# Optimization experiments

Hardware: AMD Instinct MI355X
Metric: run time of the kernel (lower is better)

Reference implementation:

```python
import jax, jax.numpy as jnp
import numpy as np

NUM_HEADS = 8  # from init_kwargs


def setup_inputs() -> dict:
    key = jax.random.key(0)
    ks = jax.random.split(key, 8)
    B, N, Din, H, Dout, E = 4, 2048, 256, 512, 256, 65536
    s = 0.02
    return {
        "x": jax.random.normal(ks[0], (B, N, Din), jnp.float32),
        "edge_index": jax.random.randint(ks[1], (2, E), 0, N),
        "W_gcn": jax.random.normal(ks[2], (Din, H), jnp.float32) * s,
        "b_gcn": jnp.zeros((H,), jnp.float32),
        "in_proj_w": jax.random.normal(ks[3], (3 * H, H), jnp.float32) * s,
        "in_proj_b": jnp.zeros((3 * H,), jnp.float32),
        "out_proj_w": jax.random.normal(ks[4], (H, H), jnp.float32) * s,
        "out_proj_b": jnp.zeros((H,), jnp.float32),
        "fc_w": jax.random.normal(ks[5], (H, Dout), jnp.float32) * s,
        "fc_b": jnp.zeros((Dout,), jnp.float32),
    }


def _gcn(x, edge_index, W, b):
    # PyG GCNConv: add self-loops, symmetric normalization, gather-scatter aggregation.
    B, N, _ = x.shape
    loop = jnp.arange(N)
    src = jnp.concatenate([edge_index[0], loop])  # message source j
    dst = jnp.concatenate([edge_index[1], loop])  # aggregation target i
    deg = jnp.zeros((N,), x.dtype).at[dst].add(1.0)
    dinv = jnp.where(deg > 0, jax.lax.rsqrt(deg), 0.0)
    norm = dinv[src] * dinv[dst]                  # [Etot]
    xl = x @ W                                    # [B, N, H]
    msgs = xl[:, src, :] * norm[None, :, None]    # [B, Etot, H]
    out = jnp.zeros_like(xl).at[:, dst].add(msgs)  # scatter-add over edges
    return out + b


def _mha(x_nbh, wi, bi, wo, bo, nh):
    # torch MultiheadAttention, input [N(seq), B, H], self-attention.
    N, B, H = x_nbh.shape
    dh = H // nh
    qkv = x_nbh @ wi.T + bi                       # [N, B, 3H]
    q, k, v = jnp.split(qkv, 3, axis=-1)
    q = q.reshape(N, B, nh, dh) * (dh ** -0.5)
    k = k.reshape(N, B, nh, dh)
    v = v.reshape(N, B, nh, dh)
    scores = jnp.einsum("nbhd,mbhd->bhnm", q, k)  # [B, nh, N, N]
    attn = jax.nn.softmax(scores, axis=-1)
    o = jnp.einsum("bhnm,mbhd->nbhd", attn, v).reshape(N, B, H)
    return o @ wo.T + bo


def reference(x, edge_index, W_gcn, b_gcn, in_proj_w, in_proj_b,
              out_proj_w, out_proj_b, fc_w, fc_b):
    h = _gcn(x, edge_index, W_gcn, b_gcn)         # [B, N, H]
    h = jnp.transpose(h, (1, 0, 2))               # [N, B, H]
    h = _mha(h, in_proj_w, in_proj_b, out_proj_w, out_proj_b, NUM_HEADS)
    h = jnp.transpose(h, (1, 0, 2))               # [B, N, H]
    h = jax.nn.relu(h)
    return h @ fc_w + fc_b                        # [B, N, Dout]
```

## Files before the change

### kernel.cpp

```cpp
#include <hip/hip_runtime.h>
#include <hip/hip_bf16.h>


#define NN 2048
#define HH 512
#define NHEAD 8
#define DH 64

typedef _Float16 f16;
typedef __attribute__((ext_vector_type(2))) _Float16 f16x2;
typedef __attribute__((ext_vector_type(4))) _Float16 f16x4;
typedef __attribute__((ext_vector_type(8))) _Float16 f16x8;
typedef __attribute__((ext_vector_type(4))) float f32x4;

#define GLOAD_LDS16(g, l)                                              \
  __builtin_amdgcn_global_load_lds(                                    \
      (const __attribute__((address_space(1))) void*)(g),              \
      (__attribute__((address_space(3))) void*)(l), 16, 0, 0)

__device__ __forceinline__ float fast_exp2(float x) {
#if __has_builtin(__builtin_amdgcn_exp2f)
  return __builtin_amdgcn_exp2f(x);
#else
  return exp2f(x);
#endif
}

__device__ __forceinline__ f16x2 cvt_pk_f16(float a, float b) {
#if __has_builtin(__builtin_amdgcn_cvt_pkrtz)
  return __builtin_bit_cast(f16x2, __builtin_amdgcn_cvt_pkrtz(a, b));
#else
  f16x2 r = { (f16)a, (f16)b };
  return r;
#endif
}


__global__ __launch_bounds__(256) void prep_all_kernel(const float* __restrict__ wi,
                                                       const float* __restrict__ wo,
                                                       const float* __restrict__ wg,
                                                       const float* __restrict__ fcw,
                                                       f16* __restrict__ wi16,
                                                       f16* __restrict__ wo16,
                                                       f16* __restrict__ wg16t,
                                                       f16* __restrict__ fcw16t,
                                                       float* __restrict__ deg,
                                                       int* __restrict__ cursor) {
  __shared__ float tbuf[32][33];
  const int bid = blockIdx.x, t = threadIdx.x;
  if (bid < 768) {
    const int i = bid * 256 + t;
    const float4 v = ((const float4*)wi)[i];
    f16x4 o = { (f16)v.x, (f16)v.y, (f16)v.z, (f16)v.w };
    ((f16x4*)wi16)[i] = o;
  } else if (bid < 1024) {
    const int i = (bid - 768) * 256 + t;
    const float4 v = ((const float4*)wo)[i];
    f16x4 o = { (f16)v.x, (f16)v.y, (f16)v.z, (f16)v.w };
    ((f16x4*)wo16)[i] = o;
  } else if (bid == 1024) {
    for (int i = t; i < NN; i += 256) { deg[i] = 0.0f; cursor[i] = 0; }
  } else {
    const int id = bid - 1025;
    const float* in;
    f16* outp;
    int R, C, bx, by;
    if (id < 128) { in = wg;  outp = wg16t;  R = 256; C = 512;
                    bx = id & 15; by = id >> 4; }
    else { int id2 = id - 128; in = fcw; outp = fcw16t; R = 512; C = 256;
           bx = id2 & 7; by = id2 >> 3; }
    const int c0 = bx * 32, r0 = by * 32;
    const int tx = t & 31, ty = t >> 5;
#pragma unroll
    for (int i = 0; i < 32; i += 8) tbuf[ty + i][tx] = in[(size_t)(r0 + ty + i) * C + c0 + tx];
    __syncthreads();
#pragma unroll
    for (int i = 0; i < 32; i += 8)
      outp[(size_t)(c0 + ty + i) * R + r0 + tx] = (f16)tbuf[tx][ty + i];
  }
}


__global__ __launch_bounds__(256) void count_deg_kernel(const int* __restrict__ ei, int E,
                                                        float* __restrict__ deg) {
  int e = blockIdx.x * 256 + threadIdx.x;
  if (e < E) atomicAdd(&deg[ei[E + e]], 1.0f);
}

__global__ __launch_bounds__(1024) void build_rowptr_kernel(const float* __restrict__ deg,
                                                            float* __restrict__ dinv,
                                                            int* __restrict__ rowptr) {
  __shared__ int a[NN];
  __shared__ int bbuf[NN];
  const int t = threadIdx.x;
  for (int i = t; i < NN; i += 1024) {
    float dg = deg[i];
    a[i] = (int)dg;
    dinv[i] = rsqrtf(dg + 1.0f);
  }
  __syncthreads();
  int* src = a;
  int* dst = bbuf;
  for (int off = 1; off < NN; off <<= 1) {
    for (int i = t; i < NN; i += 1024) {
      int v = src[i];
      if (i >= off) v += src[i - off];
      dst[i] = v;
    }
    __syncthreads();
    int* tmp = src; src = dst; dst = tmp;
  }
  for (int i = t; i < NN; i += 1024) rowptr[i + 1] = src[i];
  if (t == 0) rowptr[0] = 0;
}

__global__ __launch_bounds__(256) void fill_csr_kernel(const int* __restrict__ ei, int E,
                                                       const int* __restrict__ rowptr,
                                                       int* __restrict__ cursor,
                                                       int* __restrict__ csr_src) {
  int e = blockIdx.x * 256 + threadIdx.x;
  if (e < E) {
    int s = ei[e];
    int d = ei[E + e];
    int pos = atomicAdd(&cursor[d], 1);
    csr_src[rowptr[d] + pos] = s;
  }
}


template <int OUTMODE, bool BIAS, bool RELU, bool AF32, int MT = 128>
__global__ __launch_bounds__(256) void mfma_gemm_kernel(
    const void* __restrict__ Ap, const f16* __restrict__ Bt,
    const float* __restrict__ bias, void* __restrict__ Cout,
    int M, int N, int K,
    f16* __restrict__ q_out, f16* __restrict__ k_out, f16* __restrict__ v_out) {
  constexpr int MI = MT / 32;
  __shared__ f16 As[MT * 32];
  __shared__ f16 Bs[128 * 32];
  const int tid = threadIdx.x;
  const int wave = tid >> 6, lane = tid & 63;
  const int quad = lane >> 4, l16 = lane & 15;
  const int m0 = blockIdx.y * MT, n0 = blockIdx.x * 128;
  const int moff = (wave >> 1) * (MI * 16), noff = (wave & 1) * 64;

  f32x4 acc[MI][4];
#pragma unroll
  for (int i = 0; i < MI; ++i)
#pragma unroll
    for (int j = 0; j < 4; ++j) acc[i][j] = (f32x4){0.f, 0.f, 0.f, 0.f};

  const int rpw = MT / 4;
  const int srowA = rpw * wave + (lane >> 2);
  const int srowB = 32 * wave + (lane >> 2);
  const int kch = (lane & 3) * 8;
  const f16* Ag = (const f16*)Ap + (size_t)(m0 + srowA) * K + kch;
  const float* Ag32 = (const float*)Ap + (size_t)(m0 + srowA) * K + kch;
  const f16* Bg = Bt + (size_t)(n0 + srowB) * K + kch;
  f16* As_w = &As[(rpw * wave) * 32];
  f16* Bs_w = &Bs[(32 * wave) * 32];

  for (int k0 = 0; k0 < K; k0 += 32) {
    __syncthreads();
    if (AF32) {
#pragma unroll
      for (int t = 0; t < 2; ++t) {
        const float* g = Ag32 + k0 + (size_t)(16 * t) * K;
        const float4 u0 = *(const float4*)g;
        const float4 u1 = *(const float4*)(g + 4);
        f16x8 o = { (f16)u0.x, (f16)u0.y, (f16)u0.z, (f16)u0.w,
                    (f16)u1.x, (f16)u1.y, (f16)u1.z, (f16)u1.w };
        *(f16x8*)&As[(srowA + 16 * t) * 32 + kch] = o;
      }
    } else {
      GLOAD_LDS16(Ag + k0, As_w);
      if (MT == 128) GLOAD_LDS16(Ag + k0 + (size_t)16 * K, As_w + 16 * 32);
    }
    GLOAD_LDS16(Bg + k0, Bs_w);
    GLOAD_LDS16(Bg + k0 + (size_t)16 * K, Bs_w + 16 * 32);
    __syncthreads();
    f16x8 af[MI], bf[4];
#pragma unroll
    for (int m16 = 0; m16 < MI; ++m16)
      af[m16] = *(const f16x8*)&As[(moff + m16 * 16 + l16) * 32 + quad * 8];
#pragma unroll
    for (int n16 = 0; n16 < 4; ++n16)
      bf[n16] = *(const f16x8*)&Bs[(noff + n16 * 16 + l16) * 32 + quad * 8];
#pragma unroll
    for (int m16 = 0; m16 < MI; ++m16)
#pragma unroll
      for (int n16 = 0; n16 < 4; ++n16)
        acc[m16][n16] =
            __builtin_amdgcn_mfma_f32_16x16x32_f16(af[m16], bf[n16], acc[m16][n16], 0, 0, 0);
  }

  float bv[4];
#pragma unroll
  for (int n16 = 0; n16 < 4; ++n16)
    bv[n16] = BIAS ? bias[n0 + noff + n16 * 16 + l16] : 0.f;

  if (OUTMODE == 2) {
    const int hblk = (n0 >> 6) + (wave & 1);
    const int which = hblk >> 3, h = hblk & 7;
    f16* dst = (which == 0) ? q_out : (which == 1) ? k_out : v_out;
    const float scale = (which == 0) ? 0.125f * 1.44269504088896340736f : 1.0f;
#pragma unroll
    for (int m16 = 0; m16 < MI; ++m16) {
#pragma unroll
      for (int r = 0; r < 4; ++r) {
        const int m = m0 + moff + m16 * 16 + quad * 4 + r;
        const int b = m >> 11, ns = m & 2047;
        f16* row = dst + ((size_t)(b * 8 + h) * NN + ns) * DH;
#pragma unroll
        for (int n16 = 0; n16 < 4; ++n16) {
          const int d = n16 * 16 + l16;
          row[d] = (f16)((acc[m16][n16][r] + bv[n16]) * scale);
        }
      }
    }
  } else {
#pragma unroll
    for (int m16 = 0; m16 < MI; ++m16) {
#pragma unroll
      for (int r = 0; r < 4; ++r) {
        const size_t row = (size_t)(m0 + moff + m16 * 16 + quad * 4 + r) * N;
#pragma unroll
        for (int n16 = 0; n16 < 4; ++n16) {
          const int col = n0 + noff + n16 * 16 + l16;
          float v = acc[m16][n16][r] + bv[n16];
          if (RELU) v = fmaxf(v, 0.f);
          if (OUTMODE == 0) ((float*)Cout)[row + col] = v;
          else ((f16*)Cout)[row + col] = (f16)v;
        }
      }
    }
  }
}


__global__ __launch_bounds__(256) void gcn_aggregate_kernel(const f16* __restrict__ xl,
                                                            const float* __restrict__ dinv,
                                                            const int* __restrict__ rowptr,
                                                            const int* __restrict__ csr_src,
                                                            const float* __restrict__ b_gcn,
                                                            f16* __restrict__ out) {
  __shared__ int s_src[256];
  __shared__ float s_dv[256];
  const int i = blockIdx.x;
  const int tid = threadIdx.x;
  const float dv_i = dinv[i];
  const int b = tid >> 6;
  const int f = (tid & 63) * 8;
  const f16* xb = xl + (size_t)(b * NN) * HH + f;
  float acc[8];
  {
    const f16x8 self = *(const f16x8*)&xb[(size_t)i * HH];
#pragma unroll
    for (int j = 0; j < 8; ++j) acc[j] = (float)self[j] * dv_i;
  }
  const int beg = rowptr[i], end = rowptr[i + 1];
  for (int c0 = beg; c0 < end; c0 += 256) {
    const int cnt = min(256, end - c0);
    __syncthreads();
    if (tid < cnt) {
      int s = csr_src[c0 + tid];
      s_src[tid] = s;
      s_dv[tid] = dinv[s];
    }
    __syncthreads();
    for (int t = 0; t < cnt; ++t) {
      const f16x8 v = *(const f16x8*)&xb[(size_t)s_src[t] * HH];
      const float w = s_dv[t];
#pragma unroll
      for (int j = 0; j < 8; ++j) acc[j] = fmaf((float)v[j], w, acc[j]);
    }
  }
  const float4 bg0 = *(const float4*)&b_gcn[f];
  const float4 bg1 = *(const float4*)&b_gcn[f + 4];
  f16x8 o;
  o[0] = (f16)(acc[0] * dv_i + bg0.x);
  o[1] = (f16)(acc[1] * dv_i + bg0.y);
  o[2] = (f16)(acc[2] * dv_i + bg0.z);
  o[3] = (f16)(acc[3] * dv_i + bg0.w);
  o[4] = (f16)(acc[4] * dv_i + bg1.x);
  o[5] = (f16)(acc[5] * dv_i + bg1.y);
  o[6] = (f16)(acc[6] * dv_i + bg1.z);
  o[7] = (f16)(acc[7] * dv_i + bg1.w);
  *(f16x8*)&out[((size_t)(b * NN) + i) * HH + f] = o;
}


__global__ __launch_bounds__(512) void flash_attn_f16_kernel(const f16* __restrict__ Qb,
                                                             const f16* __restrict__ Kb,
                                                             const f16* __restrict__ Vb,
                                                             f16* __restrict__ out) {
  constexpr int LDK = 72;
  constexpr int LDV = 128;
  __shared__ f16 Ks[2][128 * LDK];
  __shared__ f16 Vt[2][64 * LDV];
  const int tid = threadIdx.x;
  const int wave = tid >> 6, lane = tid & 63;
  const int quad = lane >> 4, l16 = lane & 15;
  const int bid = blockIdx.x;
  const int sw = (bid & 7) * 64 + (bid >> 3);
  const int bh = sw >> 4;
  const int n0 = (sw & 15) * 128;
  const int b = bh >> 3, h = bh & 7;
  const f16* kb = Kb + (size_t)bh * NN * DH;
  const f16* vb = Vb + (size_t)bh * NN * DH;

  f16x8 aq0, aq1;
  {
    const f16* qf = Qb + ((size_t)bh * NN + n0 + wave * 16 + l16) * DH + quad * 8;
    aq0 = *(const f16x8*)qf;
    aq1 = *(const f16x8*)(qf + 32);
  }

  float l_part = 0.f;
  f32x4 acc_o[4];
#pragma unroll
  for (int n16 = 0; n16 < 4; ++n16) acc_o[n16] = (f32x4){0.f, 0.f, 0.f, 0.f};

  const int krow = tid >> 3, kcol = (tid & 7) * 8;
  const int vdg = tid & 15, jb = tid >> 4;
  const int vch = (jb >> 3) * 4 + (jb & 3);
  const int vrem = ((jb >> 2) & 1) * 4;
  int fdr[4];
#pragma unroll
  for (int n16 = 0; n16 < 4; ++n16)
    fdr[n16] = (2 * n16 + l16 + (l16 >> 3)) & 7;

  f16x8 kreg0, kreg1;
  f16x4 vreg[4];

  auto load_tile = [&](int k0) {
    kreg0 = *(const f16x8*)(kb + (size_t)(k0 + krow) * DH + kcol);
    kreg1 = *(const f16x8*)(kb + (size_t)(k0 + 64 + krow) * DH + kcol);
#pragma unroll
    for (int i = 0; i < 4; ++i)
      vreg[i] = *(const f16x4*)(vb + (size_t)(k0 + jb * 4 + i) * DH + vdg * 4);
  };
  auto store_tile = [&](int buf) {
    *(f16x8*)&Ks[buf][krow * LDK + kcol] = kreg0;
    *(f16x8*)&Ks[buf][(64 + krow) * LDK + kcol] = kreg1;
#pragma unroll
    for (int c = 0; c < 4; ++c) {
      const int d = vdg * 4 + c;
      const int fd = (d + (d >> 3)) & 7;
      const int off = (((vch & 8) | ((vch ^ fd) & 7)) << 3) + vrem;
      f16x4 o = { vreg[0][c], vreg[1][c], vreg[2][c], vreg[3][c] };
      *(f16x4*)&Vt[buf][d * LDV + off] = o;
    }
  };
  auto do_p = [&](int p, int cur) {
    const f16* KsC = &Ks[cur][0];
    const f16* VtC = &Vt[cur][0];
    f32x4 sA[2];
#pragma unroll
    for (int t = 0; t < 2; ++t) {
      const f16x8 ak0 = *(const f16x8*)&KsC[(p * 32 + t * 16 + l16) * LDK + quad * 8];
      const f16x8 ak1 = *(const f16x8*)&KsC[(p * 32 + t * 16 + l16) * LDK + quad * 8 + 32];
      f32x4 s = {0.f, 0.f, 0.f, 0.f};
      s = __builtin_amdgcn_mfma_f32_16x16x32_f16(ak0, aq0, s, 0, 0, 0);
      s = __builtin_amdgcn_mfma_f32_16x16x32_f16(ak1, aq1, s, 0, 0, 0);
      sA[t] = s;
    }
    f16x8 bvv[4];
    const int chp = p * 4 + quad;
#pragma unroll
    for (int n16 = 0; n16 < 4; ++n16) {
      const int off = ((chp & 8) | ((chp ^ fdr[n16]) & 7)) << 3;
      bvv[n16] = *(const f16x8*)&VtC[(n16 * 16 + l16) * LDV + off];
    }
    union { f16x8 v; f16x2 hh[4]; } ap;
    float sum = 0.f;
#pragma unroll
    for (int t = 0; t < 2; ++t)
#pragma unroll
      for (int rr = 0; rr < 2; ++rr) {
        const float e0 = fast_exp2(sA[t][rr * 2]);
        const float e1 = fast_exp2(sA[t][rr * 2 + 1]);
        sum += e0 + e1;
        ap.hh[t * 2 + rr] = cvt_pk_f16(e0, e1);
      }
    l_part += sum;
#pragma unroll
    for (int n16 = 0; n16 < 4; ++n16)
      acc_o[n16] = __builtin_amdgcn_mfma_f32_16x16x32_f16(ap.v, bvv[n16], acc_o[n16], 0, 0, 0);
  };

  load_tile(0);
  store_tile(0);
  int cur = 0;
  for (int kt = 0; kt < NN / 128; ++kt) {
    __syncthreads();
    const bool pf = (kt + 1) < (NN / 128);
    if (pf) load_tile((kt + 1) * 128);
    do_p(0, cur);
    do_p(1, cur);
    if (pf) store_tile(cur ^ 1);
    do_p(2, cur);
    do_p(3, cur);
    cur ^= 1;
  }

  float lp = l_part;
  lp += __shfl_xor(lp, 16);
  lp += __shfl_xor(lp, 32);
  f16* obase = out + ((size_t)b * NN + n0 + wave * 16) * HH + h * DH;
#pragma unroll
  for (int r = 0; r < 4; ++r) {
    const float lr = __shfl(lp, (lane & 48) | (quad * 4 + r));
    const float inv = 1.0f / lr;
#pragma unroll
    for (int n16 = 0; n16 < 4; ++n16)
      obase[(size_t)(quad * 4 + r) * HH + n16 * 16 + l16] = (f16)(acc_o[n16][r] * inv);
  }
}


extern "C" void kernel_launch(void* const* d_in, const int* in_sizes, int n_in,
                              void* d_out, int out_size, void* d_ws, size_t ws_size,
                              hipStream_t stream) {
  const float* x     = (const float*)d_in[0];
  const int*   ei    = (const int*)d_in[1];
  const float* W_gcn = (const float*)d_in[2];
  const float* b_gcn = (const float*)d_in[3];
  const float* wi    = (const float*)d_in[4];
  const float* bi    = (const float*)d_in[5];
  const float* wo    = (const float*)d_in[6];
  const float* bo    = (const float*)d_in[7];
  const float* fcw   = (const float*)d_in[8];
  const float* fcb   = (const float*)d_in[9];
  float* out = (float*)d_out;
  const int E = in_sizes[1] / 2;
  const int M = 4 * NN;

  char* wsb = (char*)d_ws;
  const size_t MB = 1u << 20;
  f16* xl16   = (f16*)(wsb + 4 * MB);
  f16* hb16   = (f16*)(wsb + 12 * MB);
  f16* Qb     = (f16*)(wsb + 20 * MB);
  f16* Kb     = (f16*)(wsb + 28 * MB);
  f16* Vb     = (f16*)(wsb + 36 * MB);
  f16* attn16 = (f16*)(wsb + 44 * MB);
  f16* proj16 = (f16*)(wsb + 52 * MB);
  f16* wi16   = (f16*)(wsb + 60 * MB);
  f16* wo16   = (f16*)(wsb + 62 * MB);
  f16* wg16t  = (f16*)(wsb + 63 * MB);
  f16* fcw16t = (f16*)(wsb + 64 * MB);
  float* deg  = (float*)(wsb + 65 * MB);
  float* dinv = deg + NN;
  int* rowptr = (int*)(dinv + NN);
  int* cursor = rowptr + 2080;
  int* csr    = cursor + NN;

  prep_all_kernel<<<1281, 256, 0, stream>>>(wi, wo, W_gcn, fcw, wi16, wo16,
                                            wg16t, fcw16t, deg, cursor);

  count_deg_kernel<<<(E + 255) / 256, 256, 0, stream>>>(ei, E, deg);
  build_rowptr_kernel<<<1, 1024, 0, stream>>>(deg, dinv, rowptr);
  fill_csr_kernel<<<(E + 255) / 256, 256, 0, stream>>>(ei, E, rowptr, cursor, csr);

  mfma_gemm_kernel<1, false, false, true><<<dim3(4, 64), 256, 0, stream>>>(
      x, wg16t, nullptr, xl16, M, 512, 256, nullptr, nullptr, nullptr);
  gcn_aggregate_kernel<<<NN, 256, 0, stream>>>(xl16, dinv, rowptr, csr, b_gcn, hb16);
  mfma_gemm_kernel<2, true, false, false><<<dim3(12, 64), 256, 0, stream>>>(
      hb16, wi16, bi, nullptr, M, 1536, 512, Qb, Kb, Vb);
  flash_attn_f16_kernel<<<512, 512, 0, stream>>>(Qb, Kb, Vb, attn16);
  mfma_gemm_kernel<1, true, true, false><<<dim3(4, 64), 256, 0, stream>>>(
      attn16, wo16, bo, proj16, M, 512, 512, nullptr, nullptr, nullptr);
  mfma_gemm_kernel<0, true, false, false, 64><<<dim3(2, 128), 256, 0, stream>>>(
      proj16, fcw16t, fcb, out, M, 256, 512, nullptr, nullptr, nullptr);
}
```

Before: 245.0 us.

## Halve attention block to 4 waves each handling two query groups, single-buffer LDS

The flash attention kernel now runs 256 threads per block, with each wave processing two 16-row query groups. Each K and V fragment read from LDS is reused across both groups, halving LDS reads per FLOP. LDS drops from double to single buffering, so the loop adds an extra barrier before each tile store. Wave priority is raised around the MFMA phase. The trade-offs are higher register pressure (two accumulator sets, with launch bounds asking for 2 blocks/SM) and less overlap between loads and compute.

```diff
diff --git a/kernel.cpp b/kernel.cpp
--- a/kernel.cpp
+++ b/kernel.cpp
@@ -289,14 +289,14 @@
 }
 
 
-__global__ __launch_bounds__(512) void flash_attn_f16_kernel(const f16* __restrict__ Qb,
-                                                             const f16* __restrict__ Kb,
-                                                             const f16* __restrict__ Vb,
-                                                             f16* __restrict__ out) {
+__global__ __launch_bounds__(256, 2) void flash_attn_f16_kernel(const f16* __restrict__ Qb,
+                                                                const f16* __restrict__ Kb,
+                                                                const f16* __restrict__ Vb,
+                                                                f16* __restrict__ out) {
   constexpr int LDK = 72;
   constexpr int LDV = 128;
-  __shared__ f16 Ks[2][128 * LDK];
-  __shared__ f16 Vt[2][64 * LDV];
+  __shared__ f16 Ks[128 * LDK];
+  __shared__ f16 Vt[64 * LDV];
   const int tid = threadIdx.x;
   const int wave = tid >> 6, lane = tid & 63;
   const int quad = lane >> 4, l16 = lane & 15;
@@ -308,112 +308,136 @@
   const f16* kb = Kb + (size_t)bh * NN * DH;
   const f16* vb = Vb + (size_t)bh * NN * DH;
 
-  f16x8 aq0, aq1;
-  {
-    const f16* qf = Qb + ((size_t)bh * NN + n0 + wave * 16 + l16) * DH + quad * 8;
-    aq0 = *(const f16x8*)qf;
-    aq1 = *(const f16x8*)(qf + 32);
-  }
-
-  float l_part = 0.f;
-  f32x4 acc_o[4];
-#pragma unroll
-  for (int n16 = 0; n16 < 4; ++n16) acc_o[n16] = (f32x4){0.f, 0.f, 0.f, 0.f};
-
-  const int krow = tid >> 3, kcol = (tid & 7) * 8;
-  const int vdg = tid & 15, jb = tid >> 4;
-  const int vch = (jb >> 3) * 4 + (jb & 3);
-  const int vrem = ((jb >> 2) & 1) * 4;
+  f16x8 aq[2][2];
+#pragma unroll
+  for (int g = 0; g < 2; ++g) {
+    const f16* qf = Qb + ((size_t)bh * NN + n0 + (wave + 4 * g) * 16 + l16) * DH + quad * 8;
+    aq[g][0] = *(const f16x8*)qf;
+    aq[g][1] = *(const f16x8*)(qf + 32);
+  }
+
+  float l_part[2] = {0.f, 0.f};
+  f32x4 acc_o[2][4];
+#pragma unroll
+  for (int g = 0; g < 2; ++g)
+#pragma unroll
+    for (int n16 = 0; n16 < 4; ++n16) acc_o[g][n16] = (f32x4){0.f, 0.f, 0.f, 0.f};
+
+  const int kr = tid >> 3, kc = (tid & 7) * 8;
+  const int vdg = tid & 15, jbb = tid >> 4;
   int fdr[4];
 #pragma unroll
   for (int n16 = 0; n16 < 4; ++n16)
     fdr[n16] = (2 * n16 + l16 + (l16 >> 3)) & 7;
 
-  f16x8 kreg0, kreg1;
-  f16x4 vreg[4];
+  f16x8 kreg[4];
+  f16x4 vreg[2][4];
 
   auto load_tile = [&](int k0) {
-    kreg0 = *(const f16x8*)(kb + (size_t)(k0 + krow) * DH + kcol);
-    kreg1 = *(const f16x8*)(kb + (size_t)(k0 + 64 + krow) * DH + kcol);
 #pragma unroll
     for (int i = 0; i < 4; ++i)
-      vreg[i] = *(const f16x4*)(vb + (size_t)(k0 + jb * 4 + i) * DH + vdg * 4);
+      kreg[i] = *(const f16x8*)(kb + (size_t)(k0 + kr + 32 * i) * DH + kc);
+#pragma unroll
+    for (int cc = 0; cc < 2; ++cc) {
+      const int jb = jbb + 16 * cc;
+#pragma unroll
+      for (int i = 0; i < 4; ++i)
+        vreg[cc][i] = *(const f16x4*)(vb + (size_t)(k0 + jb * 4 + i) * DH + vdg * 4);
+    }
   };
-  auto store_tile = [&](int buf) {
-    *(f16x8*)&Ks[buf][krow * LDK + kcol] = kreg0;
-    *(f16x8*)&Ks[buf][(64 + krow) * LDK + kcol] = kreg1;
-#pragma unroll
-    for (int c = 0; c < 4; ++c) {
-      const int d = vdg * 4 + c;
-      const int fd = (d + (d >> 3)) & 7;
-      const int off = (((vch & 8) | ((vch ^ fd) & 7)) << 3) + vrem;
-      f16x4 o = { vreg[0][c], vreg[1][c], vreg[2][c], vreg[3][c] };
-      *(f16x4*)&Vt[buf][d * LDV + off] = o;
+  auto store_tile = [&]() {
+#pragma unroll
+    for (int i = 0; i < 4; ++i)
+      *(f16x8*)&Ks[(kr + 32 * i) * LDK + kc] = kreg[i];
+#pragma unroll
+    for (int cc = 0; cc < 2; ++cc) {
+      const int jb = jbb + 16 * cc;
+      const int vch = (jb >> 3) * 4 + (jb & 3);
+      const int vrem = ((jb >> 2) & 1) * 4;
+#pragma unroll
+      for (int c = 0; c < 4; ++c) {
+        const int d = vdg * 4 + c;
+        const int fd = (d + (d >> 3)) & 7;
+        const int off = (((vch & 8) | ((vch ^ fd) & 7)) << 3) + vrem;
+        f16x4 o = { vreg[cc][0][c], vreg[cc][1][c], vreg[cc][2][c], vreg[cc][3][c] };
+        *(f16x4*)&Vt[d * LDV + off] = o;
+      }
     }
   };
-  auto do_p = [&](int p, int cur) {
-    const f16* KsC = &Ks[cur][0];
-    const f16* VtC = &Vt[cur][0];
-    f32x4 sA[2];
+  auto do_p = [&](int p) {
+    f32x4 sA[2][2];
 #pragma unroll
     for (int t = 0; t < 2; ++t) {
-      const f16x8 ak0 = *(const f16x8*)&KsC[(p * 32 + t * 16 + l16) * LDK + quad * 8];
-      const f16x8 ak1 = *(const f16x8*)&KsC[(p * 32 + t * 16 + l16) * LDK + quad * 8 + 32];
-      f32x4 s = {0.f, 0.f, 0.f, 0.f};
-      s = __builtin_amdgcn_mfma_f32_16x16x32_f16(ak0, aq0, s, 0, 0, 0);
-      s = __builtin_amdgcn_mfma_f32_16x16x32_f16(ak1, aq1, s, 0, 0, 0);
-      sA[t] = s;
+      const f16x8 ak0 = *(const f16x8*)&Ks[(p * 32 + t * 16 + l16) * LDK + quad * 8];
+      const f16x8 ak1 = *(const f16x8*)&Ks[(p * 32 + t * 16 + l16) * LDK + quad * 8 + 32];
+#pragma unroll
+      for (int g = 0; g < 2; ++g) {
+        f32x4 s = {0.f, 0.f, 0.f, 0.f};
+        s = __builtin_amdgcn_mfma_f32_16x16x32_f16(ak0, aq[g][0], s, 0, 0, 0);
+        s = __builtin_amdgcn_mfma_f32_16x16x32_f16(ak1, aq[g][1], s, 0, 0, 0);
+        sA[g][t] = s;
+      }
     }
     f16x8 bvv[4];
     const int chp = p * 4 + quad;
 #pragma unroll
     for (int n16 = 0; n16 < 4; ++n16) {
       const int off = ((chp & 8) | ((chp ^ fdr[n16]) & 7)) << 3;
-      bvv[n16] = *(const f16x8*)&VtC[(n16 * 16 + l16) * LDV + off];
-    }
-    union { f16x8 v; f16x2 hh[4]; } ap;
-    float sum = 0.f;
-#pragma unroll
-    for (int t = 0; t < 2; ++t)
-#pragma unroll
-      for (int rr = 0; rr < 2; ++rr) {
-        const float e0 = fast_exp2(sA[t][rr * 2]);
-        const float e1 = fast_exp2(sA[t][rr * 2 + 1]);
-        sum += e0 + e1;
-        ap.hh[t * 2 + rr] = cvt_pk_f16(e0, e1);
-      }
-    l_part += sum;
-#pragma unroll
-    for (int n16 = 0; n16 < 4; ++n16)
-      acc_o[n16] = __builtin_amdgcn_mfma_f32_16x16x32_f16(ap.v, bvv[n16], acc_o[n16], 0, 0, 0);
+      bvv[n16] = *(const f16x8*)&Vt[(n16 * 16 + l16) * LDV + off];
+    }
+#pragma unroll
+    for (int g = 0; g < 2; ++g) {
+      union { f16x8 v; f16x2 hh[4]; } ap;
+      float sum = 0.f;
+#pragma unroll
+      for (int t = 0; t < 2; ++t)
+#pragma unroll
+        for (int rr = 0; rr < 2; ++rr) {
+          const float e0 = fast_exp2(sA[g][t][rr * 2]);
+          const float e1 = fast_exp2(sA[g][t][rr * 2 + 1]);
+          sum += e0 + e1;
+          ap.hh[t * 2 + rr] = cvt_pk_f16(e0, e1);
+        }
+      l_part[g] += sum;
+#pragma unroll
+      for (int n16 = 0; n16 < 4; ++n16)
+        acc_o[g][n16] = __builtin_amdgcn_mfma_f32_16x16x32_f16(ap.v, bvv[n16], acc_o[g][n16], 0, 0, 0);
+    }
   };
 
   load_tile(0);
-  store_tile(0);
-  int cur = 0;
+  store_tile();
+  __syncthreads();
   for (int kt = 0; kt < NN / 128; ++kt) {
-    __syncthreads();
     const bool pf = (kt + 1) < (NN / 128);
     if (pf) load_tile((kt + 1) * 128);
-    do_p(0, cur);
-    do_p(1, cur);
-    if (pf) store_tile(cur ^ 1);
-    do_p(2, cur);
-    do_p(3, cur);
-    cur ^= 1;
-  }
-
-  float lp = l_part;
-  lp += __shfl_xor(lp, 16);
-  lp += __shfl_xor(lp, 32);
-  f16* obase = out + ((size_t)b * NN + n0 + wave * 16) * HH + h * DH;
-#pragma unroll
-  for (int r = 0; r < 4; ++r) {
-    const float lr = __shfl(lp, (lane & 48) | (quad * 4 + r));
-    const float inv = 1.0f / lr;
-#pragma unroll
-    for (int n16 = 0; n16 < 4; ++n16)
-      obase[(size_t)(quad * 4 + r) * HH + n16 * 16 + l16] = (f16)(acc_o[n16][r] * inv);
+    __builtin_amdgcn_s_setprio(1);
+    do_p(0);
+    do_p(1);
+    do_p(2);
+    do_p(3);
+    __builtin_amdgcn_s_setprio(0);
+    __syncthreads();
+    if (pf) {
+      store_tile();
+      __syncthreads();
+    }
+  }
+
+#pragma unroll
+  for (int g = 0; g < 2; ++g) {
+    float lp = l_part[g];
+    lp += __shfl_xor(lp, 16);
+    lp += __shfl_xor(lp, 32);
+    f16* obase = out + ((size_t)b * NN + n0 + (wave + 4 * g) * 16) * HH + h * DH;
+#pragma unroll
+    for (int r = 0; r < 4; ++r) {
+      const float lr = __shfl(lp, (lane & 48) | (quad * 4 + r));
+      const float inv = 1.0f / lr;
+#pragma unroll
+      for (int n16 = 0; n16 < 4; ++n16)
+        obase[(size_t)(quad * 4 + r) * HH + n16 * 16 + l16] = (f16)(acc_o[g][n16][r] * inv);
+    }
   }
 }
 
@@ -466,7 +490,7 @@
   gcn_aggregate_kernel<<<NN, 256, 0, stream>>>(xl16, dinv, rowptr, csr, b_gcn, hb16);
   mfma_gemm_kernel<2, true, false, false><<<dim3(12, 64), 256, 0, stream>>>(
       hb16, wi16, bi, nullptr, M, 1536, 512, Qb, Kb, Vb);
-  flash_attn_f16_kernel<<<512, 512, 0, stream>>>(Qb, Kb, Vb, attn16);
+  flash_attn_f16_kernel<<<512, 256, 0, stream>>>(Qb, Kb, Vb, attn16);
   mfma_gemm_kernel<1, true, true, false><<<dim3(4, 64), 256, 0, stream>>>(
       attn16, wo16, bo, proj16, M, 512, 512, nullptr, nullptr, nullptr);
   mfma_gemm_kernel<0, true, false, false, 64><<<dim3(2, 128), 256, 0, stream>>>(
```

Result: faster. 234.7 us (-4.2%).
